# Kernel tuning notes

Hardware: AMD Instinct MI355X
Metric: run time of the kernel (lower is better)

## Reference

```python
import jax, jax.numpy as jnp
import numpy as np

H = 16  # hidden_size
D = 32  # input_size == output_size
B = 2048
T = 512


def _leaky(x):
    return jnp.where(x >= 0, x, 0.01 * x)  # nn.LeakyReLU default slope


def _lstm_cell(x, h, c, Wih, Whh, bih, bhh):
    # torch.nn.LSTMCell gate order: i, f, g, o
    g = x @ Wih.T + h @ Whh.T + bih + bhh  # [B, 4H]
    i, f, gg, o = jnp.split(g, 4, axis=-1)
    i = jax.nn.sigmoid(i)
    f = jax.nn.sigmoid(f)
    gg = jnp.tanh(gg)
    o = jax.nn.sigmoid(o)
    c = f * c + i * gg
    h = o * jnp.tanh(c)
    return h, c


def setup_inputs() -> dict:
    key = jax.random.key(0)
    ks = jax.random.split(key, 20)
    s = 1.0 / np.sqrt(H)
    u = lambda k, shape: jax.random.uniform(k, shape, jnp.float32, -s, s)
    return {
        "seq": jax.random.normal(ks[0], (B, T, D), jnp.float32),
        "pre_w1": u(ks[1], (H, D)), "pre_b1": u(ks[2], (H,)),
        "pre_w2": u(ks[3], (H, H)), "pre_b2": u(ks[4], (H,)),
        "pre_w3": u(ks[5], (H, H)), "pre_b3": u(ks[6], (H,)),
        "enc_Wih": u(ks[7], (4 * H, H)), "enc_Whh": u(ks[8], (4 * H, H)),
        "enc_bih": u(ks[9], (4 * H,)), "enc_bhh": u(ks[10], (4 * H,)),
        "h2l_w1": u(ks[11], (H, H)), "h2l_b1": u(ks[12], (H,)),
        "h2l_w2": u(ks[13], (H, H)), "h2l_b2": u(ks[14], (H,)),
        "post_w": u(ks[15], (D, H)), "post_b": u(ks[16], (D,)),
    }


def reference(seq, pre_w1, pre_b1, pre_w2, pre_b2, pre_w3, pre_b3,
              enc_Wih, enc_Whh, enc_bih, enc_bhh,
              h2l_w1, h2l_b1, h2l_w2, h2l_b2, post_w, post_b):
    Bx = seq.shape[0]
    # pre MLP: Linear -> LeakyReLU -> Linear -> LeakyReLU -> Linear
    x = _leaky(seq @ pre_w1.T + pre_b1)
    x = _leaky(x @ pre_w2.T + pre_b2)
    x = x @ pre_w3.T + pre_b3  # [B, T, H]

    start0 = x[:, -1, :]
    h0 = jnp.zeros((Bx, H), seq.dtype)
    c0 = jnp.zeros((Bx, H), seq.dtype)

    # encoder loop over time (serial)
    def enc_step(carry, xt):
        h, c = carry
        h, c = _lstm_cell(xt, h, c, enc_Wih, enc_Whh, enc_bih, enc_bhh)
        return (h, c), None

    (h, c), _ = jax.lax.scan(enc_step, (h0, c0), jnp.swapaxes(x, 0, 1))

    # decoder loop (note: source reuses self.encoder cell here)
    def dec_step(carry, _):
        h, c, start = carry
        h, c = _lstm_cell(start, h, c, enc_Wih, enc_Whh, enc_bih, enc_bhh)
        start = _leaky(h @ h2l_w1.T + h2l_b1) @ h2l_w2.T + h2l_b2
        out = h @ post_w.T + post_b  # [B, D]
        return (h, c, start), out

    _, outs = jax.lax.scan(dec_step, (h, c, start0), None, length=seq.shape[1])
    # outputs[:, -1 - i] = out_i  ->  reverse time, then [B, T, D]
    outputs = jnp.swapaxes(outs[::-1], 0, 1)
    return (outputs, outputs)
```

## Files before the change

kernel.cpp:

```cpp
#include <hip/hip_runtime.h>

#define T_LEN 512
#define OSTRIDE ((size_t)2048 * 512 * 32)

typedef float v2f __attribute__((ext_vector_type(2)));
#define PKFMA(a, b, c) __builtin_elementwise_fma((a), (b), (c))

__device__ __forceinline__ float rlf(float v, int l) {
  return __int_as_float(__builtin_amdgcn_readlane(__float_as_int(v), l));
}
#define QB(v, pat) __int_as_float(__builtin_amdgcn_mov_dpp(__float_as_int(v), (pat), 0xF, 0xF, false))

__global__ __launch_bounds__(64) void setup_kernel(
    const float* __restrict__ Wih, const float* __restrict__ bih,
    const float* __restrict__ bhh, const float* __restrict__ w3,
    const float* __restrict__ b3, float* __restrict__ Wz,
    float* __restrict__ Bz) {
  const int g = threadIdx.x;
  const float sK = ((g >> 4) == 2) ? 2.0f : -1.0f;
  float acc[16];
#pragma unroll
  for (int k = 0; k < 16; ++k) acc[k] = 0.f;
  float bz = bih[g] + bhh[g];
#pragma unroll
  for (int j = 0; j < 16; ++j) {
    const float wij = Wih[g * 16 + j];
#pragma unroll
    for (int k = 0; k < 16; ++k)
      acc[k] = __builtin_fmaf(wij, w3[j * 16 + k], acc[k]);
    bz = __builtin_fmaf(wij, b3[j], bz);
  }
#pragma unroll
  for (int k = 0; k < 16; ++k) Wz[g * 16 + k] = sK * acc[k];
  Bz[g] = sK * bz;
}

__global__ __launch_bounds__(256) void prenet_y2z_kernel(
    const float* __restrict__ seq,
    const float* __restrict__ w1, const float* __restrict__ b1,
    const float* __restrict__ w2, const float* __restrict__ b2,
    const float* __restrict__ w3, const float* __restrict__ b3,
    const float* __restrict__ Wz, const float* __restrict__ Bz,
    float* __restrict__ z, float* __restrict__ xstart) {
  __shared__ float y2s[256 * 20];
  const int tid = threadIdx.x;
  const size_t rblk = (size_t)blockIdx.x * 256;
  const size_t r = rblk + tid;

  {
    const float* sp = seq + r * 32;
    float in[32];
#pragma unroll
    for (int q = 0; q < 8; ++q) {
      float4 v = ((const float4*)sp)[q];
      in[q * 4 + 0] = v.x;
      in[q * 4 + 1] = v.y;
      in[q * 4 + 2] = v.z;
      in[q * 4 + 3] = v.w;
    }

    float y1[16];
#pragma unroll
    for (int j = 0; j < 16; ++j) {
      float a0 = b1[j], a1 = 0.f, a2 = 0.f, a3 = 0.f;
#pragma unroll
      for (int k = 0; k < 32; k += 4) {
        a0 = __builtin_fmaf(w1[j * 32 + k + 0], in[k + 0], a0);
        a1 = __builtin_fmaf(w1[j * 32 + k + 1], in[k + 1], a1);
        a2 = __builtin_fmaf(w1[j * 32 + k + 2], in[k + 2], a2);
        a3 = __builtin_fmaf(w1[j * 32 + k + 3], in[k + 3], a3);
      }
      float s = (a0 + a1) + (a2 + a3);
      y1[j] = s >= 0.f ? s : 0.01f * s;
    }

    float y2[16];
#pragma unroll
    for (int j = 0; j < 16; ++j) {
      float a0 = b2[j], a1 = 0.f, a2 = 0.f, a3 = 0.f;
#pragma unroll
      for (int k = 0; k < 16; k += 4) {
        a0 = __builtin_fmaf(w2[j * 16 + k + 0], y1[k + 0], a0);
        a1 = __builtin_fmaf(w2[j * 16 + k + 1], y1[k + 1], a1);
        a2 = __builtin_fmaf(w2[j * 16 + k + 2], y1[k + 2], a2);
        a3 = __builtin_fmaf(w2[j * 16 + k + 3], y1[k + 3], a3);
      }
      float s = (a0 + a1) + (a2 + a3);
      y2[j] = s >= 0.f ? s : 0.01f * s;
    }

    float* yp = &y2s[tid * 20];
#pragma unroll
    for (int q = 0; q < 4; ++q)
      ((float4*)yp)[q] = make_float4(y2[q * 4 + 0], y2[q * 4 + 1],
                                     y2[q * 4 + 2], y2[q * 4 + 3]);

    if ((r & (T_LEN - 1)) == (T_LEN - 1)) {
      float y3[16];
#pragma unroll
      for (int j = 0; j < 16; ++j) {
        float a0 = b3[j], a1 = 0.f, a2 = 0.f, a3 = 0.f;
#pragma unroll
        for (int k = 0; k < 16; k += 4) {
          a0 = __builtin_fmaf(w3[j * 16 + k + 0], y2[k + 0], a0);
          a1 = __builtin_fmaf(w3[j * 16 + k + 1], y2[k + 1], a1);
          a2 = __builtin_fmaf(w3[j * 16 + k + 2], y2[k + 2], a2);
          a3 = __builtin_fmaf(w3[j * 16 + k + 3], y2[k + 3], a3);
        }
        y3[j] = (a0 + a1) + (a2 + a3);
      }
      float* xs = xstart + (r >> 9) * 16;
#pragma unroll
      for (int q = 0; q < 4; ++q)
        ((float4*)xs)[q] = make_float4(y3[q * 4 + 0], y3[q * 4 + 1],
                                       y3[q * 4 + 2], y3[q * 4 + 3]);
    }
  }
  __syncthreads();

  const int g = tid & 63;
  const int w = tid >> 6;

  v2f wz2[8];
  {
    const float4* wzv = (const float4*)(Wz + g * 16);
#pragma unroll
    for (int q = 0; q < 4; ++q) {
      float4 v = wzv[q];
      wz2[2 * q + 0].x = v.x;
      wz2[2 * q + 0].y = v.y;
      wz2[2 * q + 1].x = v.z;
      wz2[2 * q + 1].y = v.w;
    }
  }
  const float bz = Bz[g];

  float* zo = z + rblk * 64 + tid;
#pragma unroll 4
  for (int m = 0; m < 64; ++m) {
    const float* yp = &y2s[(4 * m + w) * 20];
    v2f A, Bv;
    A.x = bz; A.y = 0.f; Bv.x = 0.f; Bv.y = 0.f;
#pragma unroll
    for (int q = 0; q < 4; ++q) {
      float4 v = ((const float4*)yp)[q];
      v2f ylo, yhi;
      ylo.x = v.x; ylo.y = v.y; yhi.x = v.z; yhi.y = v.w;
      A = PKFMA(wz2[2 * q + 0], ylo, A);
      Bv = PKFMA(wz2[2 * q + 1], yhi, Bv);
    }
    zo[m * 256] = (A.x + A.y) + (Bv.x + Bv.y);
  }
}

#define ACTBODY()                                                           \
  do {                                                                      \
    float ee = __expf(g);                                                   \
    float rr = __builtin_amdgcn_rcpf(1.0f + ee);                            \
    float act = __builtin_fmaf(sa, rr, sb);                                 \
    float ii = QB(act, 0x00);                                               \
    float ff = QB(act, 0x55);                                               \
    float gg = QB(act, 0xAA);                                               \
    float oo = QB(act, 0xFF);                                               \
    c = __builtin_fmaf(ff, c, ii * gg);                                     \
    float th = __builtin_fmaf(                                              \
        -2.0f, __builtin_amdgcn_rcpf(1.0f + __expf(c + c)), 1.0f);          \
    h = oo * th;                                                            \
    _Pragma("unroll") for (int m = 0; m < 8; ++m) {                         \
      hk2[m].x = rlf(h, 8 * m);                                             \
      hk2[m].y = rlf(h, 8 * m + 4);                                         \
    }                                                                       \
  } while (0)

#define CELLZ(ZV)                                                           \
  do {                                                                      \
    v2f A, Bv;                                                              \
    A.x = (ZV); A.y = 0.f; Bv.x = 0.f; Bv.y = 0.f;                          \
    _Pragma("unroll") for (int m = 0; m < 8; m += 2) {                      \
      A = PKFMA(whh2[m], hk2[m], A);                                        \
      Bv = PKFMA(whh2[m + 1], hk2[m + 1], Bv);                              \
    }                                                                       \
    float g = (A.x + A.y) + (Bv.x + Bv.y);                                  \
    ACTBODY();                                                              \
  } while (0)

#define CELL(WX2, XA2, BB)                                                  \
  do {                                                                      \
    v2f A, Bv;                                                              \
    A.x = (BB); A.y = 0.f; Bv.x = 0.f; Bv.y = 0.f;                          \
    _Pragma("unroll") for (int m = 0; m < 8; m += 2) {                      \
      A = PKFMA(WX2[m], XA2[m], A);                                         \
      Bv = PKFMA(WX2[m + 1], XA2[m + 1], Bv);                               \
    }                                                                       \
    _Pragma("unroll") for (int m = 0; m < 8; m += 2) {                      \
      A = PKFMA(whh2[m], hk2[m], A);                                        \
      Bv = PKFMA(whh2[m + 1], hk2[m + 1], Bv);                              \
    }                                                                       \
    float g = (A.x + A.y) + (Bv.x + Bv.y);                                  \
    ACTBODY();                                                              \
  } while (0)

__global__ __launch_bounds__(256, 2) void lstm_rec_z_kernel(
    const float* __restrict__ Whh, const float* __restrict__ Wih,
    const float* __restrict__ bih, const float* __restrict__ bhh,
    const float* __restrict__ hw1, const float* __restrict__ hb1,
    const float* __restrict__ hw2, const float* __restrict__ hb2,
    const float* __restrict__ pw, const float* __restrict__ pb,
    const float* __restrict__ z, const float* __restrict__ xstart,
    float* __restrict__ out) {
  const int lane = threadIdx.x & 63;
  const int bu =
      __builtin_amdgcn_readfirstlane(blockIdx.x * 4 + (threadIdx.x >> 6));
  const int hr = lane >> 2;
  const int gi = (lane & 3) * 16 + hr;
  const bool isT = (lane & 3) == 2;

  const float sK = isT ? 2.0f : -1.0f;
  const float sa = isT ? -2.0f : 1.0f;
  const float sb = isT ? 1.0f : 0.0f;

  v2f whh2[8];
#pragma unroll
  for (int m = 0; m < 8; ++m) {
    whh2[m].x = Whh[gi * 16 + 2 * m + 0] * sK;
    whh2[m].y = Whh[gi * 16 + 2 * m + 1] * sK;
  }

  float h = 0.f, c = 0.f;
  v2f hk2[8];
#pragma unroll
  for (int m = 0; m < 8; ++m) { hk2[m].x = 0.f; hk2[m].y = 0.f; }

  const float* zb = z + (size_t)bu * (T_LEN * 64) + gi;
  float zq[8];
#pragma unroll
  for (int u = 0; u < 8; ++u) zq[u] = zb[(size_t)u * 64];

  for (int t0 = 0; t0 < T_LEN; t0 += 8) {
#pragma unroll
    for (int u = 0; u < 8; ++u) {
      CELLZ(zq[u]);
      int tn = t0 + u + 8;
      tn = tn < T_LEN ? tn : (T_LEN - 1);
      zq[u] = zb[(size_t)tn * 64];
    }
  }

  v2f wih2[8];
#pragma unroll
  for (int m = 0; m < 8; ++m) {
    wih2[m].x = Wih[gi * 16 + 2 * m + 0] * sK;
    wih2[m].y = Wih[gi * 16 + 2 * m + 1] * sK;
  }
  const float bias = (bih[gi] + bhh[gi]) * sK;

  const int mrow = (lane < 32) ? lane : (lane & 15);
  const float* msrc = (lane < 32) ? (pw + mrow * 16) : (hw1 + mrow * 16);
  const float mbias = (lane < 32) ? pb[mrow] : hb1[mrow];
  const float sl = (lane < 32) ? 1.0f : 0.01f;
  v2f mr2[8];
#pragma unroll
  for (int m = 0; m < 8; ++m) {
    mr2[m].x = msrc[2 * m + 0];
    mr2[m].y = msrc[2 * m + 1];
  }

  float Mr[16];
#pragma unroll
  for (int k = 0; k < 16; ++k) Mr[k] = 0.f;
#pragma unroll
  for (int j = 0; j < 16; ++j) {
    const float wj = (j & 1) ? wih2[j >> 1].y : wih2[j >> 1].x;
#pragma unroll
    for (int k = 0; k < 16; ++k)
      Mr[k] = __builtin_fmaf(wj, hw2[j * 16 + k], Mr[k]);
  }
  float mbias2 = bias;
#pragma unroll
  for (int j = 0; j < 16; ++j) {
    const float wj = (j & 1) ? wih2[j >> 1].y : wih2[j >> 1].x;
    mbias2 = __builtin_fmaf(wj, hb2[j], mbias2);
  }
  v2f Mr2[8];
#pragma unroll
  for (int m = 0; m < 8; ++m) {
    Mr2[m].x = Mr[2 * m + 0];
    Mr2[m].y = Mr[2 * m + 1];
  }

  v2f xk2[8];
  {
    const float* src = xstart + (size_t)bu * 16;
#pragma unroll
    for (int m = 0; m < 8; ++m) {
      xk2[m].x = src[2 * m + 0];
      xk2[m].y = src[2 * m + 1];
    }
  }

  const size_t obase = (size_t)bu * (T_LEN * 32) + (lane & 31);

  CELL(wih2, xk2, bias);

  for (int t = 0; t < T_LEN; ++t) {
    v2f P, Q;
    P.x = mbias; P.y = 0.f; Q.x = 0.f; Q.y = 0.f;
#pragma unroll
    for (int m = 0; m < 8; m += 2) {
      P = PKFMA(mr2[m], hk2[m], P);
      Q = PKFMA(mr2[m + 1], hk2[m + 1], Q);
    }
    float y0 = (P.x + P.y) + (Q.x + Q.y);
    float yv = fmaxf(y0, y0 * sl);

    if (lane < 32) {
      const size_t off = obase + (size_t)(T_LEN - 1 - t) * 32;
      out[off] = yv;
      out[off + OSTRIDE] = yv;
    }

    if (t + 1 < T_LEN) {
      v2f uk2[8];
#pragma unroll
      for (int m = 0; m < 8; ++m) {
        uk2[m].x = rlf(yv, 32 + 2 * m + 0);
        uk2[m].y = rlf(yv, 32 + 2 * m + 1);
      }
      CELL(Mr2, uk2, mbias2);
    }
  }
}

__device__ __forceinline__ void prenet_row(
    const float* __restrict__ sp,
    const float* __restrict__ w1, const float* __restrict__ b1,
    const float* __restrict__ w2, const float* __restrict__ b2,
    const float* __restrict__ w3, const float* __restrict__ b3,
    float y3[16]) {
  float in[32];
#pragma unroll
  for (int q = 0; q < 8; ++q) {
    float4 v = ((const float4*)sp)[q];
    in[q * 4 + 0] = v.x;
    in[q * 4 + 1] = v.y;
    in[q * 4 + 2] = v.z;
    in[q * 4 + 3] = v.w;
  }
  float y1[16];
#pragma unroll
  for (int j = 0; j < 16; ++j) {
    float a0 = b1[j], a1 = 0.f, a2 = 0.f, a3 = 0.f;
#pragma unroll
    for (int k = 0; k < 32; k += 4) {
      a0 = __builtin_fmaf(w1[j * 32 + k + 0], in[k + 0], a0);
      a1 = __builtin_fmaf(w1[j * 32 + k + 1], in[k + 1], a1);
      a2 = __builtin_fmaf(w1[j * 32 + k + 2], in[k + 2], a2);
      a3 = __builtin_fmaf(w1[j * 32 + k + 3], in[k + 3], a3);
    }
    float s = (a0 + a1) + (a2 + a3);
    y1[j] = s >= 0.f ? s : 0.01f * s;
  }
  float y2[16];
#pragma unroll
  for (int j = 0; j < 16; ++j) {
    float a0 = b2[j], a1 = 0.f, a2 = 0.f, a3 = 0.f;
#pragma unroll
    for (int k = 0; k < 16; k += 4) {
      a0 = __builtin_fmaf(w2[j * 16 + k + 0], y1[k + 0], a0);
      a1 = __builtin_fmaf(w2[j * 16 + k + 1], y1[k + 1], a1);
      a2 = __builtin_fmaf(w2[j * 16 + k + 2], y1[k + 2], a2);
      a3 = __builtin_fmaf(w2[j * 16 + k + 3], y1[k + 3], a3);
    }
    float s = (a0 + a1) + (a2 + a3);
    y2[j] = s >= 0.f ? s : 0.01f * s;
  }
#pragma unroll
  for (int j = 0; j < 16; ++j) {
    float a0 = b3[j], a1 = 0.f, a2 = 0.f, a3 = 0.f;
#pragma unroll
    for (int k = 0; k < 16; k += 4) {
      a0 = __builtin_fmaf(w3[j * 16 + k + 0], y2[k + 0], a0);
      a1 = __builtin_fmaf(w3[j * 16 + k + 1], y2[k + 1], a1);
      a2 = __builtin_fmaf(w3[j * 16 + k + 2], y2[k + 2], a2);
      a3 = __builtin_fmaf(w3[j * 16 + k + 3], y2[k + 3], a3);
    }
    y3[j] = (a0 + a1) + (a2 + a3);
  }
}

__global__ __launch_bounds__(256) void prenet_kernel(
    const float* __restrict__ seq,
    const float* __restrict__ w1, const float* __restrict__ b1,
    const float* __restrict__ w2, const float* __restrict__ b2,
    const float* __restrict__ w3, const float* __restrict__ b3,
    float* __restrict__ xws) {
  const size_t r = (size_t)blockIdx.x * 256 + threadIdx.x;
  float y3[16];
  prenet_row(seq + r * 32, w1, b1, w2, b2, w3, b3, y3);
  float* op = xws + r * 16;
#pragma unroll
  for (int q = 0; q < 4; ++q)
    ((float4*)op)[q] =
        make_float4(y3[q * 4 + 0], y3[q * 4 + 1], y3[q * 4 + 2], y3[q * 4 + 3]);
}

__global__ __launch_bounds__(256, 2) void lstm_rec_kernel(
    const float* __restrict__ Wih, const float* __restrict__ Whh,
    const float* __restrict__ bih, const float* __restrict__ bhh,
    const float* __restrict__ hw1, const float* __restrict__ hb1,
    const float* __restrict__ hw2, const float* __restrict__ hb2,
    const float* __restrict__ pw, const float* __restrict__ pb,
    const float* __restrict__ xws, float* __restrict__ out) {
  const int lane = threadIdx.x & 63;
  const int bu =
      __builtin_amdgcn_readfirstlane(blockIdx.x * 4 + (threadIdx.x >> 6));
  const int hr = lane >> 2;
  const int gi = (lane & 3) * 16 + hr;
  const bool isT = (lane & 3) == 2;

  const float sK = isT ? 2.0f : -1.0f;
  const float sa = isT ? -2.0f : 1.0f;
  const float sb = isT ? 1.0f : 0.0f;

  v2f wih2[8], whh2[8];
#pragma unroll
  for (int m = 0; m < 8; ++m) {
    wih2[m].x = Wih[gi * 16 + 2 * m + 0] * sK;
    wih2[m].y = Wih[gi * 16 + 2 * m + 1] * sK;
    whh2[m].x = Whh[gi * 16 + 2 * m + 0] * sK;
    whh2[m].y = Whh[gi * 16 + 2 * m + 1] * sK;
  }
  const float bias = (bih[gi] + bhh[gi]) * sK;

  float h = 0.f, c = 0.f;
  v2f hk2[8];
#pragma unroll
  for (int m = 0; m < 8; ++m) { hk2[m].x = 0.f; hk2[m].y = 0.f; }

  const float* xb = xws + (size_t)bu * (T_LEN * 16);

  v2f xA2[8], xB2[8];
#pragma unroll
  for (int m = 0; m < 8; ++m) {
    xA2[m].x = xb[2 * m + 0];
    xA2[m].y = xb[2 * m + 1];
  }
  for (int t = 0; t < T_LEN; t += 2) {
    const float* n1 = xb + (size_t)(t + 1) * 16;
#pragma unroll
    for (int m = 0; m < 8; ++m) {
      xB2[m].x = n1[2 * m + 0];
      xB2[m].y = n1[2 * m + 1];
    }
    CELL(wih2, xA2, bias);
    const int t2 = (t + 2 < T_LEN) ? (t + 2) : (T_LEN - 1);
    const float* n2 = xb + (size_t)t2 * 16;
#pragma unroll
    for (int m = 0; m < 8; ++m) {
      xA2[m].x = n2[2 * m + 0];
      xA2[m].y = n2[2 * m + 1];
    }
    CELL(wih2, xB2, bias);
  }

  const int mrow = (lane < 32) ? lane : (lane & 15);
  const float* msrc = (lane < 32) ? (pw + mrow * 16) : (hw1 + mrow * 16);
  const float mbias = (lane < 32) ? pb[mrow] : hb1[mrow];
  const float sl = (lane < 32) ? 1.0f : 0.01f;
  v2f mr2[8];
#pragma unroll
  for (int m = 0; m < 8; ++m) {
    mr2[m].x = msrc[2 * m + 0];
    mr2[m].y = msrc[2 * m + 1];
  }

  float Mr[16];
#pragma unroll
  for (int k = 0; k < 16; ++k) Mr[k] = 0.f;
#pragma unroll
  for (int j = 0; j < 16; ++j) {
    const float wj = (j & 1) ? wih2[j >> 1].y : wih2[j >> 1].x;
#pragma unroll
    for (int k = 0; k < 16; ++k)
      Mr[k] = __builtin_fmaf(wj, hw2[j * 16 + k], Mr[k]);
  }
  float mbias2 = bias;
#pragma unroll
  for (int j = 0; j < 16; ++j) {
    const float wj = (j & 1) ? wih2[j >> 1].y : wih2[j >> 1].x;
    mbias2 = __builtin_fmaf(wj, hb2[j], mbias2);
  }
  v2f Mr2[8];
#pragma unroll
  for (int m = 0; m < 8; ++m) {
    Mr2[m].x = Mr[2 * m + 0];
    Mr2[m].y = Mr[2 * m + 1];
  }

  v2f xk2[8];
  {
    const float* src = xb + (size_t)(T_LEN - 1) * 16;
#pragma unroll
    for (int m = 0; m < 8; ++m) {
      xk2[m].x = src[2 * m + 0];
      xk2[m].y = src[2 * m + 1];
    }
  }

  const size_t obase = (size_t)bu * (T_LEN * 32) + (lane & 31);

  CELL(wih2, xk2, bias);

  for (int t = 0; t < T_LEN; ++t) {
    v2f P, Q;
    P.x = mbias; P.y = 0.f; Q.x = 0.f; Q.y = 0.f;
#pragma unroll
    for (int m = 0; m < 8; m += 2) {
      P = PKFMA(mr2[m], hk2[m], P);
      Q = PKFMA(mr2[m + 1], hk2[m + 1], Q);
    }
    float y0 = (P.x + P.y) + (Q.x + Q.y);
    float yv = fmaxf(y0, y0 * sl);

    if (lane < 32) {
      const size_t off = obase + (size_t)(T_LEN - 1 - t) * 32;
      out[off] = yv;
      out[off + OSTRIDE] = yv;
    }

    if (t + 1 < T_LEN) {
      v2f uk2[8];
#pragma unroll
      for (int m = 0; m < 8; ++m) {
        uk2[m].x = rlf(yv, 32 + 2 * m + 0);
        uk2[m].y = rlf(yv, 32 + 2 * m + 1);
      }
      CELL(Mr2, uk2, mbias2);
    }
  }
}

extern "C" void kernel_launch(void* const* d_in, const int* in_sizes, int n_in,
                              void* d_out, int out_size, void* d_ws, size_t ws_size,
                              hipStream_t stream) {
  const float* seq = (const float*)d_in[0];
  const float* pre_w1 = (const float*)d_in[1];
  const float* pre_b1 = (const float*)d_in[2];
  const float* pre_w2 = (const float*)d_in[3];
  const float* pre_b2 = (const float*)d_in[4];
  const float* pre_w3 = (const float*)d_in[5];
  const float* pre_b3 = (const float*)d_in[6];
  const float* enc_Wih = (const float*)d_in[7];
  const float* enc_Whh = (const float*)d_in[8];
  const float* enc_bih = (const float*)d_in[9];
  const float* enc_bhh = (const float*)d_in[10];
  const float* h2l_w1 = (const float*)d_in[11];
  const float* h2l_b1 = (const float*)d_in[12];
  const float* h2l_w2 = (const float*)d_in[13];
  const float* h2l_b2 = (const float*)d_in[14];
  const float* post_w = (const float*)d_in[15];
  const float* post_b = (const float*)d_in[16];

  const size_t zbytes = (size_t)1048576 * 64 * 4;
  const size_t xsbytes = (size_t)2048 * 16 * 4;
  const size_t wzbytes = 64 * 16 * 4;
  const size_t need = zbytes + xsbytes + wzbytes + 64 * 4;

  if (ws_size >= need) {
    float* z = (float*)d_ws;
    float* xstart = (float*)((char*)d_ws + zbytes);
    float* Wz = (float*)((char*)d_ws + zbytes + xsbytes);
    float* Bz = (float*)((char*)d_ws + zbytes + xsbytes + wzbytes);

    setup_kernel<<<dim3(1), dim3(64), 0, stream>>>(
        enc_Wih, enc_bih, enc_bhh, pre_w3, pre_b3, Wz, Bz);

    prenet_y2z_kernel<<<dim3(4096), dim3(256), 0, stream>>>(
        seq, pre_w1, pre_b1, pre_w2, pre_b2, pre_w3, pre_b3, Wz, Bz, z,
        xstart);

    lstm_rec_z_kernel<<<dim3(512), dim3(256), 0, stream>>>(
        enc_Whh, enc_Wih, enc_bih, enc_bhh, h2l_w1, h2l_b1, h2l_w2, h2l_b2,
        post_w, post_b, z, xstart, (float*)d_out);
  } else {
    float* xws = (float*)d_ws;

    prenet_kernel<<<dim3(4096), dim3(256), 0, stream>>>(
        seq, pre_w1, pre_b1, pre_w2, pre_b2, pre_w3, pre_b3, xws);

    lstm_rec_kernel<<<dim3(512), dim3(256), 0, stream>>>(
        enc_Wih, enc_Whh, enc_bih, enc_bhh, h2l_w1, h2l_b1, h2l_w2, h2l_b2,
        post_w, post_b, xws, (float*)d_out);
  }
}
```

Before: 736.4 us.

## Compute encoder input projection inside recurrence from stored y2 instead of precomputed z

The prenet now writes only the 16-wide y2 activations per timestep instead of the 64-wide gate preactivation z. The recurrent kernel loads y2 rows, prefetched four steps ahead, and performs the 16x64 input projection (Wz folded with w3) inline on each step before the cell update. This cuts the intermediate workspace write and read traffic by a factor of four. In exchange it adds a per-step GEMV of packed FMAs to the serial recurrence and raises register pressure from the wz2 and prefetch buffers.

```diff
diff --git a/kernel.cpp b/kernel.cpp
--- a/kernel.cpp
+++ b/kernel.cpp
@@ -35,121 +35,81 @@
   Bz[g] = sK * bz;
 }
 
-__global__ __launch_bounds__(256) void prenet_y2z_kernel(
+__global__ __launch_bounds__(256) void prenet_y2_kernel(
     const float* __restrict__ seq,
     const float* __restrict__ w1, const float* __restrict__ b1,
     const float* __restrict__ w2, const float* __restrict__ b2,
     const float* __restrict__ w3, const float* __restrict__ b3,
-    const float* __restrict__ Wz, const float* __restrict__ Bz,
-    float* __restrict__ z, float* __restrict__ xstart) {
-  __shared__ float y2s[256 * 20];
+    float* __restrict__ y2g, float* __restrict__ xstart) {
   const int tid = threadIdx.x;
-  const size_t rblk = (size_t)blockIdx.x * 256;
-  const size_t r = rblk + tid;
-
-  {
-    const float* sp = seq + r * 32;
-    float in[32];
-#pragma unroll
-    for (int q = 0; q < 8; ++q) {
-      float4 v = ((const float4*)sp)[q];
-      in[q * 4 + 0] = v.x;
-      in[q * 4 + 1] = v.y;
-      in[q * 4 + 2] = v.z;
-      in[q * 4 + 3] = v.w;
-    }
-
-    float y1[16];
+  const size_t r = (size_t)blockIdx.x * 256 + tid;
+
+  const float* sp = seq + r * 32;
+  float in[32];
+#pragma unroll
+  for (int q = 0; q < 8; ++q) {
+    float4 v = ((const float4*)sp)[q];
+    in[q * 4 + 0] = v.x;
+    in[q * 4 + 1] = v.y;
+    in[q * 4 + 2] = v.z;
+    in[q * 4 + 3] = v.w;
+  }
+
+  float y1[16];
+#pragma unroll
+  for (int j = 0; j < 16; ++j) {
+    float a0 = b1[j], a1 = 0.f, a2 = 0.f, a3 = 0.f;
+#pragma unroll
+    for (int k = 0; k < 32; k += 4) {
+      a0 = __builtin_fmaf(w1[j * 32 + k + 0], in[k + 0], a0);
+      a1 = __builtin_fmaf(w1[j * 32 + k + 1], in[k + 1], a1);
+      a2 = __builtin_fmaf(w1[j * 32 + k + 2], in[k + 2], a2);
+      a3 = __builtin_fmaf(w1[j * 32 + k + 3], in[k + 3], a3);
+    }
+    float s = (a0 + a1) + (a2 + a3);
+    y1[j] = s >= 0.f ? s : 0.01f * s;
+  }
+
+  float y2[16];
+#pragma unroll
+  for (int j = 0; j < 16; ++j) {
+    float a0 = b2[j], a1 = 0.f, a2 = 0.f, a3 = 0.f;
+#pragma unroll
+    for (int k = 0; k < 16; k += 4) {
+      a0 = __builtin_fmaf(w2[j * 16 + k + 0], y1[k + 0], a0);
+      a1 = __builtin_fmaf(w2[j * 16 + k + 1], y1[k + 1], a1);
+      a2 = __builtin_fmaf(w2[j * 16 + k + 2], y1[k + 2], a2);
+      a3 = __builtin_fmaf(w2[j * 16 + k + 3], y1[k + 3], a3);
+    }
+    float s = (a0 + a1) + (a2 + a3);
+    y2[j] = s >= 0.f ? s : 0.01f * s;
+  }
+
+  float* op = y2g + r * 16;
+#pragma unroll
+  for (int q = 0; q < 4; ++q)
+    ((float4*)op)[q] = make_float4(y2[q * 4 + 0], y2[q * 4 + 1],
+                                   y2[q * 4 + 2], y2[q * 4 + 3]);
+
+  if ((r & (T_LEN - 1)) == (T_LEN - 1)) {
+    float y3[16];
 #pragma unroll
     for (int j = 0; j < 16; ++j) {
-      float a0 = b1[j], a1 = 0.f, a2 = 0.f, a3 = 0.f;
-#pragma unroll
-      for (int k = 0; k < 32; k += 4) {
-        a0 = __builtin_fmaf(w1[j * 32 + k + 0], in[k + 0], a0);
-        a1 = __builtin_fmaf(w1[j * 32 + k + 1], in[k + 1], a1);
-        a2 = __builtin_fmaf(w1[j * 32 + k + 2], in[k + 2], a2);
-        a3 = __builtin_fmaf(w1[j * 32 + k + 3], in[k + 3], a3);
+      float a0 = b3[j], a1 = 0.f, a2 = 0.f, a3 = 0.f;
+#pragma unroll
+      for (int k = 0; k < 16; k += 4) {
+        a0 = __builtin_fmaf(w3[j * 16 + k + 0], y2[k + 0], a0);
+        a1 = __builtin_fmaf(w3[j * 16 + k + 1], y2[k + 1], a1);
+        a2 = __builtin_fmaf(w3[j * 16 + k + 2], y2[k + 2], a2);
+        a3 = __builtin_fmaf(w3[j * 16 + k + 3], y2[k + 3], a3);
       }
-      float s = (a0 + a1) + (a2 + a3);
-      y1[j] = s >= 0.f ? s : 0.01f * s;
-    }
-
-    float y2[16];
-#pragma unroll
-    for (int j = 0; j < 16; ++j) {
-      float a0 = b2[j], a1 = 0.f, a2 = 0.f, a3 = 0.f;
-#pragma unroll
-      for (int k = 0; k < 16; k += 4) {
-        a0 = __builtin_fmaf(w2[j * 16 + k + 0], y1[k + 0], a0);
-        a1 = __builtin_fmaf(w2[j * 16 + k + 1], y1[k + 1], a1);
-        a2 = __builtin_fmaf(w2[j * 16 + k + 2], y1[k + 2], a2);
-        a3 = __builtin_fmaf(w2[j * 16 + k + 3], y1[k + 3], a3);
-      }
-      float s = (a0 + a1) + (a2 + a3);
-      y2[j] = s >= 0.f ? s : 0.01f * s;
-    }
-
-    float* yp = &y2s[tid * 20];
+      y3[j] = (a0 + a1) + (a2 + a3);
+    }
+    float* xs = xstart + (r >> 9) * 16;
 #pragma unroll
     for (int q = 0; q < 4; ++q)
-      ((float4*)yp)[q] = make_float4(y2[q * 4 + 0], y2[q * 4 + 1],
-                                     y2[q * 4 + 2], y2[q * 4 + 3]);
-
-    if ((r & (T_LEN - 1)) == (T_LEN - 1)) {
-      float y3[16];
-#pragma unroll
-      for (int j = 0; j < 16; ++j) {
-        float a0 = b3[j], a1 = 0.f, a2 = 0.f, a3 = 0.f;
-#pragma unroll
-        for (int k = 0; k < 16; k += 4) {
-          a0 = __builtin_fmaf(w3[j * 16 + k + 0], y2[k + 0], a0);
-          a1 = __builtin_fmaf(w3[j * 16 + k + 1], y2[k + 1], a1);
-          a2 = __builtin_fmaf(w3[j * 16 + k + 2], y2[k + 2], a2);
-          a3 = __builtin_fmaf(w3[j * 16 + k + 3], y2[k + 3], a3);
-        }
-        y3[j] = (a0 + a1) + (a2 + a3);
-      }
-      float* xs = xstart + (r >> 9) * 16;
-#pragma unroll
-      for (int q = 0; q < 4; ++q)
-        ((float4*)xs)[q] = make_float4(y3[q * 4 + 0], y3[q * 4 + 1],
-                                       y3[q * 4 + 2], y3[q * 4 + 3]);
-    }
-  }
-  __syncthreads();
-
-  const int g = tid & 63;
-  const int w = tid >> 6;
-
-  v2f wz2[8];
-  {
-    const float4* wzv = (const float4*)(Wz + g * 16);
-#pragma unroll
-    for (int q = 0; q < 4; ++q) {
-      float4 v = wzv[q];
-      wz2[2 * q + 0].x = v.x;
-      wz2[2 * q + 0].y = v.y;
-      wz2[2 * q + 1].x = v.z;
-      wz2[2 * q + 1].y = v.w;
-    }
-  }
-  const float bz = Bz[g];
-
-  float* zo = z + rblk * 64 + tid;
-#pragma unroll 4
-  for (int m = 0; m < 64; ++m) {
-    const float* yp = &y2s[(4 * m + w) * 20];
-    v2f A, Bv;
-    A.x = bz; A.y = 0.f; Bv.x = 0.f; Bv.y = 0.f;
-#pragma unroll
-    for (int q = 0; q < 4; ++q) {
-      float4 v = ((const float4*)yp)[q];
-      v2f ylo, yhi;
-      ylo.x = v.x; ylo.y = v.y; yhi.x = v.z; yhi.y = v.w;
-      A = PKFMA(wz2[2 * q + 0], ylo, A);
-      Bv = PKFMA(wz2[2 * q + 1], yhi, Bv);
-    }
-    zo[m * 256] = (A.x + A.y) + (Bv.x + Bv.y);
+      ((float4*)xs)[q] = make_float4(y3[q * 4 + 0], y3[q * 4 + 1],
+                                     y3[q * 4 + 2], y3[q * 4 + 3]);
   }
 }
 
@@ -200,13 +160,28 @@
     ACTBODY();                                                              \
   } while (0)
 
+#define ZGEMV(YQ, OUTV)                                                     \
+  do {                                                                      \
+    v2f A, Bv;                                                              \
+    A.x = bz; A.y = 0.f; Bv.x = 0.f; Bv.y = 0.f;                            \
+    _Pragma("unroll") for (int q = 0; q < 4; ++q) {                         \
+      float4 v = (YQ)[q];                                                   \
+      v2f ylo, yhi;                                                         \
+      ylo.x = v.x; ylo.y = v.y; yhi.x = v.z; yhi.y = v.w;                   \
+      A = PKFMA(wz2[2 * q + 0], ylo, A);                                    \
+      Bv = PKFMA(wz2[2 * q + 1], yhi, Bv);                                  \
+    }                                                                       \
+    OUTV = (A.x + A.y) + (Bv.x + Bv.y);                                     \
+  } while (0)
+
 __global__ __launch_bounds__(256, 2) void lstm_rec_z_kernel(
     const float* __restrict__ Whh, const float* __restrict__ Wih,
     const float* __restrict__ bih, const float* __restrict__ bhh,
     const float* __restrict__ hw1, const float* __restrict__ hb1,
     const float* __restrict__ hw2, const float* __restrict__ hb2,
     const float* __restrict__ pw, const float* __restrict__ pb,
-    const float* __restrict__ z, const float* __restrict__ xstart,
+    const float* __restrict__ Wz, const float* __restrict__ Bz,
+    const float* __restrict__ y2g, const float* __restrict__ xstart,
     float* __restrict__ out) {
   const int lane = threadIdx.x & 63;
   const int bu =
@@ -226,23 +201,43 @@
     whh2[m].y = Whh[gi * 16 + 2 * m + 1] * sK;
   }
 
+  v2f wz2[8];
+  {
+    const float4* wzv = (const float4*)(Wz + gi * 16);
+#pragma unroll
+    for (int q = 0; q < 4; ++q) {
+      float4 v = wzv[q];
+      wz2[2 * q + 0].x = v.x;
+      wz2[2 * q + 0].y = v.y;
+      wz2[2 * q + 1].x = v.z;
+      wz2[2 * q + 1].y = v.w;
+    }
+  }
+  const float bz = Bz[gi];
+
   float h = 0.f, c = 0.f;
   v2f hk2[8];
 #pragma unroll
   for (int m = 0; m < 8; ++m) { hk2[m].x = 0.f; hk2[m].y = 0.f; }
 
-  const float* zb = z + (size_t)bu * (T_LEN * 64) + gi;
-  float zq[8];
-#pragma unroll
-  for (int u = 0; u < 8; ++u) zq[u] = zb[(size_t)u * 64];
-
-  for (int t0 = 0; t0 < T_LEN; t0 += 8) {
-#pragma unroll
-    for (int u = 0; u < 8; ++u) {
-      CELLZ(zq[u]);
-      int tn = t0 + u + 8;
+  const float4* yb = (const float4*)(y2g + (size_t)bu * (T_LEN * 16));
+  float4 yq[4][4];
+#pragma unroll
+  for (int u = 0; u < 4; ++u) {
+#pragma unroll
+    for (int q = 0; q < 4; ++q) yq[u][q] = yb[u * 4 + q];
+  }
+
+  for (int t0 = 0; t0 < T_LEN; t0 += 4) {
+#pragma unroll
+    for (int u = 0; u < 4; ++u) {
+      float zv;
+      ZGEMV(yq[u], zv);
+      CELLZ(zv);
+      int tn = t0 + u + 4;
       tn = tn < T_LEN ? tn : (T_LEN - 1);
-      zq[u] = zb[(size_t)tn * 64];
+#pragma unroll
+      for (int q = 0; q < 4; ++q) yq[u][q] = yb[(size_t)tn * 4 + q];
     }
   }
 
@@ -561,27 +556,26 @@
   const float* post_w = (const float*)d_in[15];
   const float* post_b = (const float*)d_in[16];
 
-  const size_t zbytes = (size_t)1048576 * 64 * 4;
+  const size_t y2bytes = (size_t)2048 * 512 * 16 * 4;
   const size_t xsbytes = (size_t)2048 * 16 * 4;
   const size_t wzbytes = 64 * 16 * 4;
-  const size_t need = zbytes + xsbytes + wzbytes + 64 * 4;
+  const size_t need = y2bytes + xsbytes + wzbytes + 64 * 4;
 
   if (ws_size >= need) {
-    float* z = (float*)d_ws;
-    float* xstart = (float*)((char*)d_ws + zbytes);
-    float* Wz = (float*)((char*)d_ws + zbytes + xsbytes);
-    float* Bz = (float*)((char*)d_ws + zbytes + xsbytes + wzbytes);
+    float* y2g = (float*)d_ws;
+    float* xstart = (float*)((char*)d_ws + y2bytes);
+    float* Wz = (float*)((char*)d_ws + y2bytes + xsbytes);
+    float* Bz = (float*)((char*)d_ws + y2bytes + xsbytes + wzbytes);
 
     setup_kernel<<<dim3(1), dim3(64), 0, stream>>>(
         enc_Wih, enc_bih, enc_bhh, pre_w3, pre_b3, Wz, Bz);
 
-    prenet_y2z_kernel<<<dim3(4096), dim3(256), 0, stream>>>(
-        seq, pre_w1, pre_b1, pre_w2, pre_b2, pre_w3, pre_b3, Wz, Bz, z,
-        xstart);
+    prenet_y2_kernel<<<dim3(4096), dim3(256), 0, stream>>>(
+        seq, pre_w1, pre_b1, pre_w2, pre_b2, pre_w3, pre_b3, y2g, xstart);
 
     lstm_rec_z_kernel<<<dim3(512), dim3(256), 0, stream>>>(
         enc_Whh, enc_Wih, enc_bih, enc_bhh, h2l_w1, h2l_b1, h2l_w2, h2l_b2,
-        post_w, post_b, z, xstart, (float*)d_out);
+        post_w, post_b, Wz, Bz, y2g, xstart, (float*)d_out);
   } else {
     float* xws = (float*)d_ws;
 
```

After: 862.4 us. +17.1%, slower.
